# Optimization experiments

Hardware: AMD Instinct MI355X
Metric: run time of the kernel (lower is better)

The kernel has to match this reference:

```python
import jax, jax.numpy as jnp
import numpy as np

DIM = 1024
D_STATE = 64
D_CONV = 4
EXPAND = 2
HEADDIM = 64
D_INNER = EXPAND * DIM                      # 2048
NHEADS = D_INNER // HEADDIM                 # 32
D_CONV_DIM = D_INNER + 2 * D_STATE          # 2176 (ngroups=1)
D_IN_PROJ = 2 * D_INNER + 2 * D_STATE + NHEADS  # 4256


def setup_inputs() -> dict:
    key = jax.random.key(0)
    ks = jax.random.split(key, 9)
    B, L = 4, 2048
    x = jax.random.normal(ks[0], (B, L, DIM), dtype=jnp.float32)
    in_proj_w = jax.random.normal(ks[1], (D_IN_PROJ, DIM), dtype=jnp.float32) * 0.02
    conv_w = jax.random.normal(ks[2], (D_CONV_DIM, D_CONV), dtype=jnp.float32) * 0.2
    conv_b = jax.random.normal(ks[3], (D_CONV_DIM,), dtype=jnp.float32) * 0.02
    # dt bias from inverse-softplus of dt ~ U(1e-3, 0.1) (mamba2 init)
    dt = jnp.exp(jax.random.uniform(ks[4], (NHEADS,)) * (np.log(0.1) - np.log(1e-3)) + np.log(1e-3))
    dt_bias = (dt + jnp.log(-jnp.expm1(-dt))).astype(jnp.float32)
    A_log = jnp.log(jax.random.uniform(ks[5], (NHEADS,), minval=1.0, maxval=16.0)).astype(jnp.float32)
    D = jnp.ones((NHEADS,), dtype=jnp.float32)
    norm_w = jnp.ones((D_INNER,), dtype=jnp.float32)
    out_proj_w = jax.random.normal(ks[6], (DIM, D_INNER), dtype=jnp.float32) * 0.02
    return {"x": x, "in_proj_w": in_proj_w, "conv_w": conv_w, "conv_b": conv_b,
            "dt_bias": dt_bias, "A_log": A_log, "D": D, "norm_w": norm_w,
            "out_proj_w": out_proj_w}


def _mamba2_fwd(x, in_proj_w, conv_w, conv_b, dt_bias, A_log, D, norm_w, out_proj_w):
    B, L, _ = x.shape
    zxbcdt = jnp.einsum('bld,ed->ble', x, in_proj_w)  # (B,L,4256)
    z = zxbcdt[..., :D_INNER]
    xBC = zxbcdt[..., D_INNER:D_INNER + D_CONV_DIM]
    dt = jax.nn.softplus(zxbcdt[..., D_INNER + D_CONV_DIM:] + dt_bias)  # (B,L,H)
    # causal depthwise conv (kernel D_CONV) + silu
    xp = jnp.pad(xBC, ((0, 0), (D_CONV - 1, 0), (0, 0)))
    conv = conv_b
    for k in range(D_CONV):
        conv = conv + xp[:, k:k + L, :] * conv_w[:, k]
    xBC = jax.nn.silu(conv)
    x_ssm = xBC[..., :D_INNER].reshape(B, L, NHEADS, HEADDIM)
    Bm = xBC[..., D_INNER:D_INNER + D_STATE]          # (B,L,N) ngroups=1
    Cm = xBC[..., D_INNER + D_STATE:]                 # (B,L,N)
    A = -jnp.exp(A_log)                               # (H,)

    def step(h, inp):
        xt, Bt, Ct, dtt = inp                         # (B,H,P),(B,N),(B,N),(B,H)
        dA = jnp.exp(dtt * A)                         # (B,H)
        h = h * dA[:, :, None, None] + (dtt[:, :, None] * xt)[..., None] * Bt[:, None, None, :]
        y = jnp.einsum('bhpn,bn->bhp', h, Ct)
        return h, y

    h0 = jnp.zeros((B, NHEADS, HEADDIM, D_STATE), dtype=x.dtype)
    xs = (jnp.swapaxes(x_ssm, 0, 1), jnp.swapaxes(Bm, 0, 1),
          jnp.swapaxes(Cm, 0, 1), jnp.swapaxes(dt, 0, 1))
    _, ys = jax.lax.scan(step, h0, xs)                # (L,B,H,P)
    y = jnp.swapaxes(ys, 0, 1) + x_ssm * D[None, None, :, None]
    y = y.reshape(B, L, D_INNER)
    # gated RMSNorm (norm_before_gate=False): norm(y * silu(z))
    g = y * jax.nn.silu(z)
    g = g * jax.lax.rsqrt(jnp.mean(g * g, axis=-1, keepdims=True) + 1e-5) * norm_w
    return jnp.einsum('ble,de->bld', g, out_proj_w)


def reference(x, in_proj_w, conv_w, conv_b, dt_bias, A_log, D, norm_w, out_proj_w):
    return _mamba2_fwd(x, in_proj_w, conv_w, conv_b, dt_bias, A_log, D, norm_w, out_proj_w)
```

## Files before the change

### kernel.cpp

```cpp
#include <hip/hip_runtime.h>
#include <stdint.h>

typedef unsigned short ushort_t;
typedef __attribute__((ext_vector_type(4))) float f32x4;
typedef __attribute__((ext_vector_type(8))) short short8;
typedef __attribute__((ext_vector_type(4))) unsigned short us4;

#define L_SEQ   2048
#define NROWS   8192
#define KDIM    1024
#define DINNER  2048
#define NHEADS  32
#define DSTATE  64
#define DCONVD  2176
#define NPROJ   4256
#define NPROJP  4352
#define LDZX    4352
#define NCHUNK  32

__device__ __forceinline__ float bf2f(ushort_t u) {
    union { uint32_t i; float f; } v; v.i = ((uint32_t)u) << 16; return v.f;
}
__device__ __forceinline__ ushort_t f2bf(float f) {
    uint32_t x = __float_as_uint(f);
    x += 0x7FFFu + ((x >> 16) & 1u);
    return (ushort_t)(x >> 16);
}
__device__ __forceinline__ int swzi(int row, int col) {
    return row * 64 + (col ^ ((row & 7) << 3));
}

__global__ __launch_bounds__(256) void cast_bf16_kernel(const float* __restrict__ in,
                                                        ushort_t* __restrict__ out, int n4) {
    int i = blockIdx.x * 256 + threadIdx.x;
    if (i >= n4) return;
    float4 v = ((const float4*)in)[i];
    ushort4 o;
    o.x = f2bf(v.x); o.y = f2bf(v.y); o.z = f2bf(v.z); o.w = f2bf(v.w);
    ((ushort4*)out)[i] = o;
}

__global__ __launch_bounds__(256) void cast_pad_w_kernel(const float* __restrict__ w,
                                                         ushort_t* __restrict__ out) {
    int i = blockIdx.x * 256 + threadIdx.x;
    int idx = i * 4;
    int row = idx >> 10;
    ushort4 o;
    if (row < NPROJ) {
        float4 v = ((const float4*)w)[i];
        o.x = f2bf(v.x); o.y = f2bf(v.y); o.z = f2bf(v.z); o.w = f2bf(v.w);
    } else {
        o.x = 0; o.y = 0; o.z = 0; o.w = 0;
    }
    ((ushort4*)out)[i] = o;
}

__device__ __forceinline__ void async16(const void* g, void* l) {
    __builtin_amdgcn_global_load_lds((const __attribute__((address_space(1))) void*)g,
                                     (__attribute__((address_space(3))) void*)l, 16, 0, 0);
}

template<int BN, bool OUT_BF16>
__global__ __launch_bounds__(512, 1) void gemm256_kernel(const ushort_t* __restrict__ Ap,
                                                         const ushort_t* __restrict__ Bp,
                                                         void* __restrict__ Cp,
                                                         const int K, const int ldc,
                                                         const int ntn) {
    constexpr int FC = BN / 64;
    constexpr int LB = BN / 128;
    constexpr int VN = 2 + LB;
    __shared__ ushort_t ldsA[2][2][256 * 32];
    __shared__ ushort_t ldsB[2][2][BN * 32];

    const int tid = threadIdx.x;
    const int w = tid >> 6, l = tid & 63;
    const int lr = l & 15, lk = l >> 4;
    const int wm = w >> 2, wn = w & 3;

    const int lin = blockIdx.x;
    const int cpx = gridDim.x >> 3;
    const int swz = (lin & 7) * cpx + (lin >> 3);
    const int nt = swz % ntn, mt = swz / ntn;
    const int m0 = mt * 256, n0 = nt * BN;
    const int bcol = wn * (BN / 4);

    const int sr0 = tid >> 2,         sg0 = (tid & 3) ^ (sr0 & 3) ^ ((sr0 >> 2) & 3);
    const int sr1 = (512 + tid) >> 2, sg1 = ((512 + tid) & 3) ^ (sr1 & 3) ^ ((sr1 >> 2) & 3);

    f32x4 acc[8][FC];
    const f32x4 zero = {0.f, 0.f, 0.f, 0.f};
#pragma unroll
    for (int i = 0; i < 8; ++i)
#pragma unroll
        for (int j = 0; j < FC; ++j) acc[i][j] = zero;

    auto stageA = [&](int d_, int kh, int ktn) {
        const ushort_t* gb = Ap + (size_t)m0 * K + (size_t)ktn * 64 + kh * 32;
        async16(gb + (size_t)sr0 * K + sg0 * 8, (ushort_t*)&ldsA[d_][kh][0] + tid * 8);
        async16(gb + (size_t)sr1 * K + sg1 * 8, (ushort_t*)&ldsA[d_][kh][0] + (512 + tid) * 8);
    };
    auto stageB = [&](int d_, int kh, int ktn) {
        const ushort_t* gb = Bp + (size_t)n0 * K + (size_t)ktn * 64 + kh * 32;
        async16(gb + (size_t)sr0 * K + sg0 * 8, (ushort_t*)&ldsB[d_][kh][0] + tid * 8);
        if constexpr (LB == 2)
            async16(gb + (size_t)sr1 * K + sg1 * 8, (ushort_t*)&ldsB[d_][kh][0] + (512 + tid) * 8);
    };

#define VMWAIT_VN do { if constexpr (VN == 4) asm volatile("s_waitcnt vmcnt(4)" ::: "memory"); \
                       else                   asm volatile("s_waitcnt vmcnt(3)" ::: "memory"); } while (0)
#define VMWAIT_0  asm volatile("s_waitcnt vmcnt(0)" ::: "memory")

    short8 bfv[FC];

#define PHASE(ks_, frh_, STAGE_STMT, VM_STMT) do {                                      \
        short8 af[4];                                                                   \
        _Pragma("unroll")                                                               \
        for (int fr = 0; fr < 4; ++fr) {                                                \
            const int row = wm * 128 + ((frh_) * 4 + fr) * 16 + lr;                     \
            const int sl = lk ^ (row & 3) ^ ((row >> 2) & 3);                           \
            af[fr] = *(const short8*)&ldsA[d][ks_][row * 32 + sl * 8];                  \
        }                                                                               \
        if ((frh_) == 0) {                                                              \
            _Pragma("unroll")                                                           \
            for (int fc = 0; fc < FC; ++fc) {                                           \
                const int row = bcol + fc * 16 + lr;                                    \
                const int sl = lk ^ (row & 3) ^ ((row >> 2) & 3);                       \
                bfv[fc] = *(const short8*)&ldsB[d][ks_][row * 32 + sl * 8];             \
            }                                                                           \
        }                                                                               \
        STAGE_STMT;                                                                     \
        __builtin_amdgcn_s_barrier();                                                   \
        __builtin_amdgcn_s_setprio(1);                                                  \
        _Pragma("unroll")                                                               \
        for (int fr = 0; fr < 4; ++fr)                                                  \
            _Pragma("unroll")                                                           \
            for (int fc = 0; fc < FC; ++fc)                                             \
                acc[(frh_) * 4 + fr][fc] = __builtin_amdgcn_mfma_f32_16x16x32_bf16(     \
                    af[fr], bfv[fc], acc[(frh_) * 4 + fr][fc], 0, 0, 0);                \
        __builtin_amdgcn_s_setprio(0);                                                  \
        VM_STMT;                                                                        \
        __builtin_amdgcn_s_barrier();                                                   \
    } while (0)

    stageA(0, 0, 0); stageB(0, 0, 0);
    stageA(0, 1, 0); stageB(0, 1, 0);
    VMWAIT_VN;
    __builtin_amdgcn_s_barrier();

    const int NKT = K >> 6;
    for (int kt = 0; kt < NKT; ++kt) {
        const int d = kt & 1;
        const bool more = (kt + 1 < NKT);
        PHASE(0, 0, { if (more) stageA(d ^ 1, 0, kt + 1); }, {});
        PHASE(0, 1, { if (more) stageB(d ^ 1, 0, kt + 1); },
                    { if (more) VMWAIT_VN; else VMWAIT_0; });
        PHASE(1, 0, { if (more) stageA(d ^ 1, 1, kt + 1); }, {});
        PHASE(1, 1, { if (more) stageB(d ^ 1, 1, kt + 1); },
                    { if (more) VMWAIT_VN; });
    }
#undef PHASE
#undef VMWAIT_VN
#undef VMWAIT_0

#pragma unroll
    for (int fr2 = 0; fr2 < 8; ++fr2)
#pragma unroll
        for (int fc2 = 0; fc2 < FC; ++fc2) {
            const int col = n0 + bcol + fc2 * 16 + lr;
            const int rowb = m0 + wm * 128 + fr2 * 16 + lk * 4;
#pragma unroll
            for (int r = 0; r < 4; ++r) {
                if (OUT_BF16)
                    ((ushort_t*)Cp)[(size_t)(rowb + r) * ldc + col] = f2bf(acc[fr2][fc2][r]);
                else
                    ((float*)Cp)[(size_t)(rowb + r) * ldc + col] = acc[fr2][fc2][r];
            }
        }
}

__global__ __launch_bounds__(256) void conv_silu_kernel(const ushort_t* __restrict__ zx,
                                                        const float* __restrict__ conv_w,
                                                        const float* __restrict__ conv_b,
                                                        ushort_t* __restrict__ convout) {
    const int idx = blockIdx.x * 256 + threadIdx.x;
    const int row = idx / 272;
    const int c = (idx - row * 272) * 8;
    const int l = row & (L_SEQ - 1);
    float acc[8];
    {
        const float4* bp = (const float4*)(conv_b + c);
        float4 b0 = bp[0], b1 = bp[1];
        acc[0] = b0.x; acc[1] = b0.y; acc[2] = b0.z; acc[3] = b0.w;
        acc[4] = b1.x; acc[5] = b1.y; acc[6] = b1.z; acc[7] = b1.w;
    }
    float wv[8][4];
    {
        const float4* wp = (const float4*)(conv_w + c * 4);
#pragma unroll
        for (int i = 0; i < 8; ++i) {
            float4 t = wp[i];
            wv[i][0] = t.x; wv[i][1] = t.y; wv[i][2] = t.z; wv[i][3] = t.w;
        }
    }
#pragma unroll
    for (int k = 0; k < 4; ++k) {
        const int ll = l - 3 + k;
        if (ll >= 0) {
            short8 v = *(const short8*)(zx + (size_t)(row - 3 + k) * LDZX + DINNER + c);
#pragma unroll
            for (int i = 0; i < 8; ++i)
                acc[i] += bf2f((ushort_t)v[i]) * wv[i][k];
        }
    }
    short8 o;
#pragma unroll
    for (int i = 0; i < 8; ++i) {
        float s = acc[i] / (1.f + expf(-acc[i]));
        o[i] = (short)f2bf(s);
    }
    *(short8*)(convout + (size_t)row * DCONVD + c) = o;
}

__global__ __launch_bounds__(256) void chunk_intra_kernel(
    const ushort_t* __restrict__ cvb, const ushort_t* __restrict__ zx,
    const float* __restrict__ dt_bias,
    const float* __restrict__ A_log, const float* __restrict__ Dvec,
    ushort_t* __restrict__ ybuf, ushort_t* __restrict__ Gbuf,
    float* __restrict__ expPb)
{
    const int c = blockIdx.x, h = blockIdx.y, b = blockIdx.z;
    const int tid = threadIdx.x;
    const int wv = tid >> 6, lane = tid & 63;
    const int lr = lane & 15, lk = lane >> 4;

    __shared__ __align__(16) ushort_t Cs[4096];
    __shared__ __align__(16) ushort_t Bs[4096];
    __shared__ __align__(16) ushort_t Xt[4096];
    __shared__ __align__(16) ushort_t Ss[4096];
    __shared__ __align__(16) ushort_t Bw[4096];
    __shared__ float sP[64], sdt[64], sWf[64];

    const int t4 = tid >> 2, qq = tid & 3;
    const size_t rowg0 = (size_t)b * L_SEQ + c * 64;
    const ushort_t* rowp = cvb + (rowg0 + t4) * DCONVD;

    short8 rb0 = *(const short8*)(rowp + DINNER + qq * 16);
    short8 rb1 = *(const short8*)(rowp + DINNER + qq * 16 + 8);
    short8 rc0 = *(const short8*)(rowp + DINNER + DSTATE + qq * 16);
    short8 rc1 = *(const short8*)(rowp + DINNER + DSTATE + qq * 16 + 8);
    short8 rx0 = *(const short8*)(rowp + h * 64 + qq * 16);
    short8 rx1 = *(const short8*)(rowp + h * 64 + qq * 16 + 8);

    *(short8*)&Cs[swzi(t4, qq * 16)]     = rc0;
    *(short8*)&Cs[swzi(t4, qq * 16 + 8)] = rc1;
    *(short8*)&Bs[swzi(t4, qq * 16)]     = rb0;
    *(short8*)&Bs[swzi(t4, qq * 16 + 8)] = rb1;
#pragma unroll
    for (int k = 0; k < 8; ++k) {
        Xt[swzi(qq * 16 + k, t4)]     = (ushort_t)rx0[k];
        Xt[swzi(qq * 16 + 8 + k, t4)] = (ushort_t)rx1[k];
    }
    if (tid < 64) {
        float dv = bf2f(zx[(rowg0 + tid) * LDZX + (NPROJ - NHEADS) + h]) + dt_bias[h];
        float dt = (dv > 20.f) ? dv : log1pf(expf(dv));
        float A = -__expf(A_log[h]);
        float P = dt * A;
#pragma unroll
        for (int off = 1; off < 64; off <<= 1) {
            float o = __shfl_up(P, off);
            if (tid >= off) P += o;
        }
        sP[tid] = P;
        sdt[tid] = dt;
        float P63 = __shfl(P, 63);
        sWf[tid] = __expf(P63 - P) * dt;
        expPb[(size_t)(b * NHEADS + h) * L_SEQ + c * 64 + tid] = __expf(P);
    }
    __syncthreads();

    {
        const float w = sWf[t4];
#pragma unroll
        for (int k = 0; k < 8; ++k) {
            Bw[swzi(qq * 16 + k, t4)]     = f2bf(bf2f((ushort_t)rb0[k]) * w);
            Bw[swzi(qq * 16 + 8 + k, t4)] = f2bf(bf2f((ushort_t)rb1[k]) * w);
        }
    }

    const float Dh = Dvec[h];
    {
        short8 a0 = *(const short8*)&Cs[swzi(wv * 16 + lr, lk * 8)];
        short8 a1 = *(const short8*)&Cs[swzi(wv * 16 + lr, 32 + lk * 8)];
        f32x4 acc[4];
        const f32x4 zero = {0.f, 0.f, 0.f, 0.f};
#pragma unroll
        for (int nj = 0; nj < 4; ++nj) {
            short8 b0 = *(const short8*)&Bs[swzi(nj * 16 + lr, lk * 8)];
            short8 b1 = *(const short8*)&Bs[swzi(nj * 16 + lr, 32 + lk * 8)];
            acc[nj] = __builtin_amdgcn_mfma_f32_16x16x32_bf16(a0, b0, zero, 0, 0, 0);
            acc[nj] = __builtin_amdgcn_mfma_f32_16x16x32_bf16(a1, b1, acc[nj], 0, 0, 0);
        }
#pragma unroll
        for (int r = 0; r < 4; ++r) {
            const int i = wv * 16 + lk * 4 + r;
            const float Pi = sP[i];
#pragma unroll
            for (int nj = 0; nj < 4; ++nj) {
                const int j = nj * 16 + lr;
                float s = 0.f;
                if (j <= i) s = acc[nj][r] * __expf(Pi - sP[j]) * sdt[j];
                if (j == i) s += Dh;
                Ss[swzi(i, j)] = f2bf(s);
            }
        }
    }
    __syncthreads();

    {
        short8 a0 = *(const short8*)&Ss[swzi(wv * 16 + lr, lk * 8)];
        short8 a1 = *(const short8*)&Ss[swzi(wv * 16 + lr, 32 + lk * 8)];
        const f32x4 zero = {0.f, 0.f, 0.f, 0.f};
#pragma unroll
        for (int np = 0; np < 4; ++np) {
            short8 b0 = *(const short8*)&Xt[swzi(np * 16 + lr, lk * 8)];
            short8 b1 = *(const short8*)&Xt[swzi(np * 16 + lr, 32 + lk * 8)];
            f32x4 acc = __builtin_amdgcn_mfma_f32_16x16x32_bf16(a0, b0, zero, 0, 0, 0);
            acc = __builtin_amdgcn_mfma_f32_16x16x32_bf16(a1, b1, acc, 0, 0, 0);
#pragma unroll
            for (int r = 0; r < 4; ++r) {
                const int i = wv * 16 + lk * 4 + r;
                const int p = np * 16 + lr;
                ybuf[(rowg0 + i) * DINNER + (size_t)h * 64 + p] = f2bf(acc[r]);
            }
        }
    }

    {
        short8 a0 = *(const short8*)&Xt[swzi(wv * 16 + lr, lk * 8)];
        short8 a1 = *(const short8*)&Xt[swzi(wv * 16 + lr, 32 + lk * 8)];
        const f32x4 zero = {0.f, 0.f, 0.f, 0.f};
        const size_t gbase = ((size_t)((b * NHEADS + h) * NCHUNK + c)) << 12;
#pragma unroll
        for (int nt = 0; nt < 4; ++nt) {
            short8 b0 = *(const short8*)&Bw[swzi(nt * 16 + lr, lk * 8)];
            short8 b1 = *(const short8*)&Bw[swzi(nt * 16 + lr, 32 + lk * 8)];
            f32x4 acc = __builtin_amdgcn_mfma_f32_16x16x32_bf16(a0, b0, zero, 0, 0, 0);
            acc = __builtin_amdgcn_mfma_f32_16x16x32_bf16(a1, b1, acc, 0, 0, 0);
#pragma unroll
            for (int r = 0; r < 4; ++r) {
                const int p = wv * 16 + lk * 4 + r;
                const int n = nt * 16 + lr;
                Gbuf[gbase + p * 64 + n] = f2bf(acc[r]);
            }
        }
    }
}

__global__ __launch_bounds__(256) void state_scan_kernel(
    ushort_t* __restrict__ GH, const float* __restrict__ expPb)
{
    const int half = blockIdx.x, h = blockIdx.y, b = blockIdx.z;
    const int bh = b * NHEADS + h;
    const int e0 = half * 2048 + threadIdx.x * 8;
    ushort_t* base = GH + ((size_t)bh << 17);
    const float* ep = expPb + (size_t)bh * L_SEQ;

    float hr[8];
#pragma unroll
    for (int k = 0; k < 8; ++k) hr[k] = 0.f;

    short8 g = *(const short8*)(base + e0);
    float Ec = ep[63];
    for (int c = 0; c < NCHUNK; ++c) {
        short8 gn = g; float En = 0.f;
        if (c + 1 < NCHUNK) {
            gn = *(const short8*)(base + ((size_t)(c + 1) << 12) + e0);
            En = ep[(c + 1) * 64 + 63];
        }
        short8 o;
#pragma unroll
        for (int k = 0; k < 8; ++k) o[k] = (short)f2bf(hr[k]);
        *(short8*)(base + ((size_t)c << 12) + e0) = o;
#pragma unroll
        for (int k = 0; k < 8; ++k) hr[k] = hr[k] * Ec + bf2f((ushort_t)g[k]);
        g = gn; Ec = En;
    }
}

__global__ __launch_bounds__(256) void y_inter_kernel(
    const ushort_t* __restrict__ cvb, const float* __restrict__ expPb,
    const ushort_t* __restrict__ hst, ushort_t* __restrict__ ybuf)
{
    const int c = blockIdx.x + 1, h = blockIdx.y, b = blockIdx.z;
    const int tid = threadIdx.x;
    const int wv = tid >> 6, lane = tid & 63;
    const int lr = lane & 15, lk = lane >> 4;
    const int bh = b * NHEADS + h;

    __shared__ __align__(16) ushort_t Cs[4096];
    __shared__ __align__(16) ushort_t Hp[4096];
    __shared__ float sEp[64];

    const int t4 = tid >> 2, qq = tid & 3;
    const size_t rowg0 = (size_t)b * L_SEQ + c * 64;
    {
        const ushort_t* rp = cvb + (rowg0 + t4) * DCONVD + DINNER + DSTATE + qq * 16;
        *(short8*)&Cs[swzi(t4, qq * 16)]     = *(const short8*)rp;
        *(short8*)&Cs[swzi(t4, qq * 16 + 8)] = *(const short8*)(rp + 8);
        const ushort_t* hr = hst + (((size_t)(bh * NCHUNK + c)) << 12) + t4 * 64 + qq * 16;
        *(short8*)&Hp[swzi(t4, qq * 16)]     = *(const short8*)hr;
        *(short8*)&Hp[swzi(t4, qq * 16 + 8)] = *(const short8*)(hr + 8);
    }
    if (tid < 64) sEp[tid] = expPb[(size_t)bh * L_SEQ + c * 64 + tid];
    __syncthreads();

    short8 a0 = *(const short8*)&Cs[swzi(wv * 16 + lr, lk * 8)];
    short8 a1 = *(const short8*)&Cs[swzi(wv * 16 + lr, 32 + lk * 8)];
    const f32x4 zero = {0.f, 0.f, 0.f, 0.f};
#pragma unroll
    for (int np = 0; np < 4; ++np) {
        short8 b0 = *(const short8*)&Hp[swzi(np * 16 + lr, lk * 8)];
        short8 b1 = *(const short8*)&Hp[swzi(np * 16 + lr, 32 + lk * 8)];
        f32x4 acc = __builtin_amdgcn_mfma_f32_16x16x32_bf16(a0, b0, zero, 0, 0, 0);
        acc = __builtin_amdgcn_mfma_f32_16x16x32_bf16(a1, b1, acc, 0, 0, 0);
#pragma unroll
        for (int r = 0; r < 4; ++r) {
            const int t = wv * 16 + lk * 4 + r;
            const int p = np * 16 + lr;
            ushort_t* yp = &ybuf[(rowg0 + t) * DINNER + (size_t)h * 64 + p];
            *yp = f2bf(bf2f(*yp) + acc[r] * sEp[t]);
        }
    }
}

__global__ __launch_bounds__(256) void gatenorm_kernel(const ushort_t* __restrict__ ybuf,
                                                       const ushort_t* __restrict__ zx,
                                                       const float* __restrict__ norm_w,
                                                       ushort_t* __restrict__ gbuf) {
    const int row = blockIdx.x;
    const int tid = threadIdx.x;
    short8 yv = *(const short8*)(ybuf + (size_t)row * DINNER + tid * 8);
    short8 zv = *(const short8*)(zx + (size_t)row * LDZX + tid * 8);
    float g[8];
    float ss = 0.f;
#pragma unroll
    for (int i = 0; i < 8; ++i) {
        float y = bf2f((ushort_t)yv[i]);
        float z = bf2f((ushort_t)zv[i]);
        float sz = z / (1.f + expf(-z));
        float gg = y * sz;
        g[i] = gg;
        ss += gg * gg;
    }
#pragma unroll
    for (int o = 32; o > 0; o >>= 1) ss += __shfl_xor(ss, o);
    __shared__ float wsum[4];
    if ((tid & 63) == 0) wsum[tid >> 6] = ss;
    __syncthreads();
    float tot = wsum[0] + wsum[1] + wsum[2] + wsum[3];
    float scale = rsqrtf(tot * (1.0f / (float)DINNER) + 1e-5f);
    short8 o8;
#pragma unroll
    for (int i = 0; i < 8; ++i)
        o8[i] = (short)f2bf(g[i] * scale * norm_w[tid * 8 + i]);
    *(short8*)(gbuf + (size_t)row * DINNER + tid * 8) = o8;
}

extern "C" void kernel_launch(void* const* d_in, const int* in_sizes, int n_in,
                              void* d_out, int out_size, void* d_ws, size_t ws_size,
                              hipStream_t stream) {
    const float* x          = (const float*)d_in[0];
    const float* in_proj_w  = (const float*)d_in[1];
    const float* conv_w     = (const float*)d_in[2];
    const float* conv_b     = (const float*)d_in[3];
    const float* dt_bias    = (const float*)d_in[4];
    const float* A_log      = (const float*)d_in[5];
    const float* Dvec       = (const float*)d_in[6];
    const float* norm_w     = (const float*)d_in[7];
    const float* out_proj_w = (const float*)d_in[8];
    float* out = (float*)d_out;

    char* ws = (char*)d_ws;
    size_t off = 0;
    ushort_t* owbf  = (ushort_t*)(ws + off); off += (size_t)KDIM * DINNER * 2;
    ushort_t* zx    = (ushort_t*)(ws + off); off += (size_t)NROWS * LDZX * 2;
    ushort_t* cvb   = (ushort_t*)(ws + off); off += (size_t)NROWS * DCONVD * 2;
    float*    expPb = (float*)(ws + off);    off += (size_t)128 * L_SEQ * 4;
    ushort_t* ybuf  = (ushort_t*)(ws + off); off += (size_t)NROWS * DINNER * 2;
    char* tail = ws + off;
    ushort_t* xbf  = (ushort_t*)tail;
    ushort_t* wbf  = (ushort_t*)(tail + (size_t)NROWS * KDIM * 2);
    ushort_t* Gbuf = (ushort_t*)tail;
    ushort_t* gbuf = (ushort_t*)tail;

    cast_bf16_kernel<<<8192, 256, 0, stream>>>(x, xbf, NROWS * KDIM / 4);
    cast_pad_w_kernel<<<4352, 256, 0, stream>>>(in_proj_w, wbf);
    cast_bf16_kernel<<<2048, 256, 0, stream>>>(out_proj_w, owbf, KDIM * DINNER / 4);

    gemm256_kernel<256, true><<<544, 512, 0, stream>>>(xbf, wbf, zx, KDIM, LDZX, 17);

    conv_silu_kernel<<<NROWS * 272 / 256, 256, 0, stream>>>(zx, conv_w, conv_b, cvb);

    chunk_intra_kernel<<<dim3(NCHUNK, NHEADS, 4), 256, 0, stream>>>(
        cvb, zx, dt_bias, A_log, Dvec, ybuf, Gbuf, expPb);
    state_scan_kernel<<<dim3(2, NHEADS, 4), 256, 0, stream>>>(Gbuf, expPb);
    y_inter_kernel<<<dim3(NCHUNK - 1, NHEADS, 4), 256, 0, stream>>>(
        cvb, expPb, Gbuf, ybuf);

    gatenorm_kernel<<<NROWS, 256, 0, stream>>>(ybuf, zx, norm_w, gbuf);

    gemm256_kernel<128, false><<<256, 512, 0, stream>>>(gbuf, owbf, out, DINNER, KDIM, 8);
}
```

Baseline: 325.7 us.

## Replace 256-row GEMM with 128x128 tile kernel at two blocks per CU

Both projection GEMMs move from a 512-thread kernel with 256xBN tiles and a four-phase pipeline to a 256-thread 128x128 tile kernel with launch bounds allowing two blocks per CU. The k-step is 64 in a single LDS buffer per stage with an XOR swizzle, and there are fewer barriers per iteration. The aim is more blocks in flight and simpler synchronization, with latency hidden through occupancy. The cost is lower per-block data reuse from the smaller tiles, so more global and LDS traffic per flop.

```diff
diff --git a/kernel.cpp b/kernel.cpp
--- a/kernel.cpp
+++ b/kernel.cpp
@@ -60,114 +60,100 @@
                                      (__attribute__((address_space(3))) void*)l, 16, 0, 0);
 }
 
-template<int BN, bool OUT_BF16>
-__global__ __launch_bounds__(512, 1) void gemm256_kernel(const ushort_t* __restrict__ Ap,
+template<bool OUT_BF16>
+__global__ __launch_bounds__(256, 2) void gemm128_kernel(const ushort_t* __restrict__ Ap,
                                                          const ushort_t* __restrict__ Bp,
                                                          void* __restrict__ Cp,
                                                          const int K, const int ldc,
                                                          const int ntn) {
-    constexpr int FC = BN / 64;
-    constexpr int LB = BN / 128;
-    constexpr int VN = 2 + LB;
-    __shared__ ushort_t ldsA[2][2][256 * 32];
-    __shared__ ushort_t ldsB[2][2][BN * 32];
-
+    __shared__ ushort_t ldsA[2][8192];
+    __shared__ ushort_t ldsB[2][8192];
     const int tid = threadIdx.x;
     const int w = tid >> 6, l = tid & 63;
     const int lr = l & 15, lk = l >> 4;
-    const int wm = w >> 2, wn = w & 3;
+    const int wm = w >> 1, wn = w & 1;
 
     const int lin = blockIdx.x;
     const int cpx = gridDim.x >> 3;
     const int swz = (lin & 7) * cpx + (lin >> 3);
     const int nt = swz % ntn, mt = swz / ntn;
-    const int m0 = mt * 256, n0 = nt * BN;
-    const int bcol = wn * (BN / 4);
-
-    const int sr0 = tid >> 2,         sg0 = (tid & 3) ^ (sr0 & 3) ^ ((sr0 >> 2) & 3);
-    const int sr1 = (512 + tid) >> 2, sg1 = ((512 + tid) & 3) ^ (sr1 & 3) ^ ((sr1 >> 2) & 3);
-
-    f32x4 acc[8][FC];
+    const int m0 = mt * 128, n0 = nt * 128;
+
+    int srow[4], scol[4];
+#pragma unroll
+    for (int i = 0; i < 4; ++i) {
+        int s = i * 256 + tid;
+        srow[i] = s >> 3;
+        scol[i] = (s & 7) ^ (srow[i] & 7);
+    }
+
+    f32x4 acc[4][4];
     const f32x4 zero = {0.f, 0.f, 0.f, 0.f};
 #pragma unroll
-    for (int i = 0; i < 8; ++i)
-#pragma unroll
-        for (int j = 0; j < FC; ++j) acc[i][j] = zero;
-
-    auto stageA = [&](int d_, int kh, int ktn) {
-        const ushort_t* gb = Ap + (size_t)m0 * K + (size_t)ktn * 64 + kh * 32;
-        async16(gb + (size_t)sr0 * K + sg0 * 8, (ushort_t*)&ldsA[d_][kh][0] + tid * 8);
-        async16(gb + (size_t)sr1 * K + sg1 * 8, (ushort_t*)&ldsA[d_][kh][0] + (512 + tid) * 8);
+    for (int i = 0; i < 4; ++i)
+#pragma unroll
+        for (int j = 0; j < 4; ++j) acc[i][j] = zero;
+
+    auto stageA = [&](int d_, int ktn) {
+        const ushort_t* gb = Ap + (size_t)m0 * K + (size_t)ktn * 64;
+#pragma unroll
+        for (int i = 0; i < 4; ++i)
+            async16(gb + (size_t)srow[i] * K + scol[i] * 8, &ldsA[d_][(i * 256 + tid) * 8]);
     };
-    auto stageB = [&](int d_, int kh, int ktn) {
-        const ushort_t* gb = Bp + (size_t)n0 * K + (size_t)ktn * 64 + kh * 32;
-        async16(gb + (size_t)sr0 * K + sg0 * 8, (ushort_t*)&ldsB[d_][kh][0] + tid * 8);
-        if constexpr (LB == 2)
-            async16(gb + (size_t)sr1 * K + sg1 * 8, (ushort_t*)&ldsB[d_][kh][0] + (512 + tid) * 8);
+    auto stageB = [&](int d_, int ktn) {
+        const ushort_t* gb = Bp + (size_t)n0 * K + (size_t)ktn * 64;
+#pragma unroll
+        for (int i = 0; i < 4; ++i)
+            async16(gb + (size_t)srow[i] * K + scol[i] * 8, &ldsB[d_][(i * 256 + tid) * 8]);
     };
 
-#define VMWAIT_VN do { if constexpr (VN == 4) asm volatile("s_waitcnt vmcnt(4)" ::: "memory"); \
-                       else                   asm volatile("s_waitcnt vmcnt(3)" ::: "memory"); } while (0)
-#define VMWAIT_0  asm volatile("s_waitcnt vmcnt(0)" ::: "memory")
-
-    short8 bfv[FC];
-
-#define PHASE(ks_, frh_, STAGE_STMT, VM_STMT) do {                                      \
-        short8 af[4];                                                                   \
+#define CKS(ks_) do {                                                                   \
+        short8 af[4], bfv[4];                                                           \
         _Pragma("unroll")                                                               \
         for (int fr = 0; fr < 4; ++fr) {                                                \
-            const int row = wm * 128 + ((frh_) * 4 + fr) * 16 + lr;                     \
-            const int sl = lk ^ (row & 3) ^ ((row >> 2) & 3);                           \
-            af[fr] = *(const short8*)&ldsA[d][ks_][row * 32 + sl * 8];                  \
+            const int ar = wm * 64 + fr * 16 + lr;                                      \
+            af[fr] = *(const short8*)&ldsA[d][ar * 64 + ((((ks_) * 4 + lk) ^ (ar & 7)) << 3)]; \
         }                                                                               \
-        if ((frh_) == 0) {                                                              \
-            _Pragma("unroll")                                                           \
-            for (int fc = 0; fc < FC; ++fc) {                                           \
-                const int row = bcol + fc * 16 + lr;                                    \
-                const int sl = lk ^ (row & 3) ^ ((row >> 2) & 3);                       \
-                bfv[fc] = *(const short8*)&ldsB[d][ks_][row * 32 + sl * 8];             \
-            }                                                                           \
+        _Pragma("unroll")                                                               \
+        for (int fc = 0; fc < 4; ++fc) {                                                \
+            const int br = wn * 64 + fc * 16 + lr;                                      \
+            bfv[fc] = *(const short8*)&ldsB[d][br * 64 + ((((ks_) * 4 + lk) ^ (br & 7)) << 3)]; \
         }                                                                               \
-        STAGE_STMT;                                                                     \
-        __builtin_amdgcn_s_barrier();                                                   \
         __builtin_amdgcn_s_setprio(1);                                                  \
         _Pragma("unroll")                                                               \
         for (int fr = 0; fr < 4; ++fr)                                                  \
             _Pragma("unroll")                                                           \
-            for (int fc = 0; fc < FC; ++fc)                                             \
-                acc[(frh_) * 4 + fr][fc] = __builtin_amdgcn_mfma_f32_16x16x32_bf16(     \
-                    af[fr], bfv[fc], acc[(frh_) * 4 + fr][fc], 0, 0, 0);                \
+            for (int fc = 0; fc < 4; ++fc)                                              \
+                acc[fr][fc] = __builtin_amdgcn_mfma_f32_16x16x32_bf16(                  \
+                    af[fr], bfv[fc], acc[fr][fc], 0, 0, 0);                             \
         __builtin_amdgcn_s_setprio(0);                                                  \
-        VM_STMT;                                                                        \
-        __builtin_amdgcn_s_barrier();                                                   \
     } while (0)
 
-    stageA(0, 0, 0); stageB(0, 0, 0);
-    stageA(0, 1, 0); stageB(0, 1, 0);
-    VMWAIT_VN;
+    stageA(0, 0); stageB(0, 0);
+    asm volatile("s_waitcnt vmcnt(0)" ::: "memory");
     __builtin_amdgcn_s_barrier();
 
     const int NKT = K >> 6;
     for (int kt = 0; kt < NKT; ++kt) {
         const int d = kt & 1;
         const bool more = (kt + 1 < NKT);
-        PHASE(0, 0, { if (more) stageA(d ^ 1, 0, kt + 1); }, {});
-        PHASE(0, 1, { if (more) stageB(d ^ 1, 0, kt + 1); },
-                    { if (more) VMWAIT_VN; else VMWAIT_0; });
-        PHASE(1, 0, { if (more) stageA(d ^ 1, 1, kt + 1); }, {});
-        PHASE(1, 1, { if (more) stageB(d ^ 1, 1, kt + 1); },
-                    { if (more) VMWAIT_VN; });
-    }
-#undef PHASE
-#undef VMWAIT_VN
-#undef VMWAIT_0
-
-#pragma unroll
-    for (int fr2 = 0; fr2 < 8; ++fr2)
-#pragma unroll
-        for (int fc2 = 0; fc2 < FC; ++fc2) {
-            const int col = n0 + bcol + fc2 * 16 + lr;
-            const int rowb = m0 + wm * 128 + fr2 * 16 + lk * 4;
+        if (more) stageA(d ^ 1, kt + 1);
+        if (more) asm volatile("s_waitcnt vmcnt(4)" ::: "memory");
+        else      asm volatile("s_waitcnt vmcnt(0)" ::: "memory");
+        __builtin_amdgcn_s_barrier();
+        CKS(0);
+        if (more) stageB(d ^ 1, kt + 1);
+        CKS(1);
+        __builtin_amdgcn_s_barrier();
+    }
+#undef CKS
+
+#pragma unroll
+    for (int fr2 = 0; fr2 < 4; ++fr2)
+#pragma unroll
+        for (int fc2 = 0; fc2 < 4; ++fc2) {
+            const int col = n0 + wn * 64 + fc2 * 16 + lr;
+            const int rowb = m0 + wm * 64 + fr2 * 16 + lk * 4;
 #pragma unroll
             for (int r = 0; r < 4; ++r) {
                 if (OUT_BF16)
@@ -497,7 +483,7 @@
     cast_pad_w_kernel<<<4352, 256, 0, stream>>>(in_proj_w, wbf);
     cast_bf16_kernel<<<2048, 256, 0, stream>>>(out_proj_w, owbf, KDIM * DINNER / 4);
 
-    gemm256_kernel<256, true><<<544, 512, 0, stream>>>(xbf, wbf, zx, KDIM, LDZX, 17);
+    gemm128_kernel<true><<<2176, 256, 0, stream>>>(xbf, wbf, zx, KDIM, LDZX, 34);
 
     conv_silu_kernel<<<NROWS * 272 / 256, 256, 0, stream>>>(zx, conv_w, conv_b, cvb);
 
@@ -509,5 +495,5 @@
 
     gatenorm_kernel<<<NROWS, 256, 0, stream>>>(ybuf, zx, norm_w, gbuf);
 
-    gemm256_kernel<128, false><<<256, 512, 0, stream>>>(gbuf, owbf, out, DINNER, KDIM, 8);
-}
+    gemm128_kernel<false><<<512, 256, 0, stream>>>(gbuf, owbf, out, DINNER, KDIM, 8);
+}
```

Measured after the change: 341.8 us. 1.05x slower.
